# Optimization experiments

Hardware: AMD Instinct MI355X
Metric: run time of the kernel (lower is better)

Reference implementation:

```python
import jax, jax.numpy as jnp
import numpy as np

N = 3600      # nodes (pinned by h0/c0 shape in the torch module)
H = 512       # lstm_hidden
PES = 588     # pes feature width (LSTM input size)
PROT = 384    # protein feature width
OC = 256      # out_channels
E = 230400    # edges (avg degree 64)


def _lstm_cell(x, h, c, wih, whh, bih, bhh):
    # single-timestep PyTorch LSTM cell; gate order i, f, g, o
    g = x @ wih.T + h @ whh.T + bih + bhh
    i, f, gg, o = jnp.split(g, 4, axis=-1)
    c2 = jax.nn.sigmoid(f) * c + jax.nn.sigmoid(i) * jnp.tanh(gg)
    return jax.nn.sigmoid(o) * jnp.tanh(c2)


def _gcn(x, rows, cols, norm, W, b):
    # PyG GCNConv: X' = D^{-1/2}(A+I)D^{-1/2} X W + b
    xw = x @ W
    return jax.ops.segment_sum(xw[rows] * norm[:, None], cols, num_segments=N) + b


def setup_inputs() -> dict:
    key = jax.random.key(0)
    ks = jax.random.split(key, 24)
    s = 0.05
    d = {
        "x": jax.random.normal(ks[0], (N, PES + PROT), jnp.float32),
        "edge_index": jax.random.randint(ks[1], (2, E), 0, N),
        "h0": jax.random.normal(ks[2], (4, N, H), jnp.float32),
        "c0": jax.random.normal(ks[3], (4, N, H), jnp.float32),
    }
    ins = [PES, PES, 2 * H, 2 * H]
    names = ["l0f", "l0b", "l1f", "l1b"]
    for i, (nm, di) in enumerate(zip(names, ins)):
        d["wih" + nm] = jax.random.normal(ks[4 + 4 * i], (4 * H, di), jnp.float32) * s
        d["whh" + nm] = jax.random.normal(ks[5 + 4 * i], (4 * H, H), jnp.float32) * s
        d["bih" + nm] = jnp.zeros((4 * H,), jnp.float32)
        d["bhh" + nm] = jnp.zeros((4 * H,), jnp.float32)
    d["W1"] = jax.random.normal(ks[20], (PROT + 2 * H, 2 * OC), jnp.float32) * s
    d["b1"] = jnp.zeros((2 * OC,), jnp.float32)
    d["W2"] = jax.random.normal(ks[21], (2 * OC, OC), jnp.float32) * s
    d["b2"] = jnp.zeros((OC,), jnp.float32)
    return d


def reference(x, edge_index, h0, c0,
              wihl0f, whhl0f, bihl0f, bhhl0f,
              wihl0b, whhl0b, bihl0b, bhhl0b,
              wihl1f, whhl1f, bihl1f, bhhl1f,
              wihl1b, whhl1b, bihl1b, bhhl1b,
              W1, b1, W2, b2):
    pes = x[:, :PES]
    prot = x[:, PES:]
    # BiLSTM over seq_len=1: one cell step per direction per layer
    hf = _lstm_cell(pes, h0[0], c0[0], wihl0f, whhl0f, bihl0f, bhhl0f)
    hb = _lstm_cell(pes, h0[1], c0[1], wihl0b, whhl0b, bihl0b, bhhl0b)
    x1 = jnp.concatenate([hf, hb], axis=1)
    hf2 = _lstm_cell(x1, h0[2], c0[2], wihl1f, whhl1f, bihl1f, bhhl1f)
    hb2 = _lstm_cell(x1, h0[3], c0[3], wihl1b, whhl1b, bihl1b, bhhl1b)
    x_p = jnp.concatenate([hf2, hb2], axis=1) / 100.0
    feat = jnp.concatenate([prot, x_p], axis=1)  # dropout is identity in eval
    # add self-loops, symmetric normalization
    loop = jnp.arange(N)
    rows = jnp.concatenate([edge_index[0], loop])
    cols = jnp.concatenate([edge_index[1], loop])
    deg = jax.ops.segment_sum(jnp.ones_like(rows, jnp.float32), cols, num_segments=N)
    dinv = jax.lax.rsqrt(deg)  # deg >= 1 because of self-loops
    norm = dinv[rows] * dinv[cols]
    h1 = jax.nn.relu(_gcn(feat, rows, cols, norm, W1, b1))
    return _gcn(h1, rows, cols, norm, W2, b2)
```

## Files before the change

kernel.cpp:

```cpp
#include <hip/hip_runtime.h>
#include <hip/hip_bf16.h>

#define NN 3600
#define MP 3712
#define KADJ 3616
#define NH (3600*512)
#define EE 230400
#define NKT0 9
#define NKT1 12

typedef __hip_bfloat16 bf16;
typedef __bf16 bf16x8 __attribute__((ext_vector_type(8)));
typedef float f32x4 __attribute__((ext_vector_type(4)));
typedef int i32x8 __attribute__((ext_vector_type(8)));
typedef unsigned char u8x16 __attribute__((ext_vector_type(16)));

typedef __attribute__((address_space(1))) void as1v;
typedef __attribute__((address_space(3))) void as3v;

__device__ __forceinline__ void glds16(void* lds, const void* g) {
  __builtin_amdgcn_global_load_lds((as1v*)(void*)g, (as3v*)lds, 16, 0, 0);
}

__device__ __forceinline__ float sigm(float v) { return 1.0f / (1.0f + expf(-v)); }

__device__ __forceinline__ unsigned char f2fp8(float f) {
  return (unsigned char)(__builtin_amdgcn_cvt_pk_fp8_f32(f, 0.f, 0, false) & 0xff);
}

template<int MODE>
__global__ __launch_bounds__(256) void gemm_lstm8(
    const unsigned char* __restrict__ Axf, const unsigned char* __restrict__ Ahf,
    const unsigned char* __restrict__ Bf,
    const float* __restrict__ c0f, const float* __restrict__ bihf,
    const float* __restrict__ bhhf,
    const unsigned char* __restrict__ Axb, const unsigned char* __restrict__ Ahb,
    const unsigned char* __restrict__ Bb,
    const float* __restrict__ c0b, const float* __restrict__ bihb,
    const float* __restrict__ bhhb,
    void* __restrict__ dst1,
    int nktx, int nkt, int hx)
{
  __shared__ alignas(16) unsigned char smem[65536];
  const int hid = (int)blockIdx.y * 32 + (int)blockIdx.x;
  const int xcd = hid & 7, idx = hid >> 3;
  int bx, by;
  if (idx < 112) { bx = (xcd & 3) * 8 + (idx & 7); by = (xcd >> 2) * 14 + (idx >> 3); }
  else { int k = idx - 112; bx = (xcd & 3) * 8 + k * 2 + (xcd >> 2); by = 28; }
  const bool back = bx >= hx;
  const unsigned char* Ax = back ? Axb : Axf;
  const unsigned char* Ah = back ? Ahb : Ahf;
  const unsigned char* B  = back ? Bb  : Bf;
  const float* c0  = back ? c0b : c0f;
  const float* bih = back ? bihb : bihf;
  const float* bhh = back ? bhhb : bhhf;
  const int t = threadIdx.x, w = t >> 6, l = t & 63;
  const int nblk = back ? bx - hx : bx;
  const unsigned char* gA  = Ax + (((size_t)by * nktx) << 14) + t*16;
  const unsigned char* gAh = Ah + (((size_t)by * (nkt - nktx)) << 14) + t*16;
  const unsigned char* gB  = B  + (((size_t)nblk * nkt) << 14) + t*16;
  const int wm = (w>>1)*64, wn = (w&1)*64;
  const int kb = l >> 4;
  const int aoff = kb*4096 + (wm + (l&15))*32;
  const int boff = 16384 + kb*4096 + (wn + (l&15))*32;
  f32x4 acc[4][4] = {};

  auto STAGE = [&](int buf, int kt) {
    unsigned char* lA = smem + buf*32768 + w*1024;
    unsigned char* lB = smem + buf*32768 + 16384 + w*1024;
    const unsigned char* srcA = (kt < nktx) ? gA + ((size_t)kt << 14)
                                            : gAh + ((size_t)(kt - nktx) << 14);
    const size_t ko = (size_t)kt << 14;
    glds16(lA,          srcA);
    glds16(lA + 4096,   srcA + 4096);
    glds16(lA + 8192,   srcA + 8192);
    glds16(lA + 12288,  srcA + 12288);
    glds16(lB,          gB + ko);
    glds16(lB + 4096,   gB + ko + 4096);
    glds16(lB + 8192,   gB + ko + 8192);
    glds16(lB + 12288,  gB + ko + 12288);
  };

  STAGE(0, 0);
  STAGE(1, 1);
  int cur = 0;
  for (int kt = 0; kt < nkt; ++kt) {
    if (kt + 1 < nkt) asm volatile("s_waitcnt vmcnt(8)" ::: "memory");
    else              asm volatile("s_waitcnt vmcnt(0)" ::: "memory");
    __builtin_amdgcn_sched_barrier(0);
    __builtin_amdgcn_s_barrier();
    __builtin_amdgcn_sched_barrier(0);
    const unsigned char* base = smem + cur*32768;
    i32x8 av[4], bv[4];
#pragma unroll
    for (int mi = 0; mi < 4; ++mi) av[mi] = *(const i32x8*)(base + aoff + mi*512);
#pragma unroll
    for (int ni = 0; ni < 4; ++ni) bv[ni] = *(const i32x8*)(base + boff + ni*512);
#pragma unroll
    for (int mi = 0; mi < 4; ++mi)
#pragma unroll
      for (int ni = 0; ni < 4; ++ni)
        acc[mi][ni] = __builtin_amdgcn_mfma_scale_f32_16x16x128_f8f6f4(
            av[mi], bv[ni], acc[mi][ni], 0, 0, 0, 127, 0, 127);
    __builtin_amdgcn_sched_barrier(0);
    __builtin_amdgcn_s_barrier();
    __builtin_amdgcn_sched_barrier(0);
    if (kt + 2 < nkt) STAGE(cur, kt + 2);
    cur ^= 1;
  }
  const int jh = (((nblk << 7) + wn) >> 2) + (l & 15);
  const float bI = bih[jh]        + bhh[jh];
  const float bF = bih[512 + jh]  + bhh[512 + jh];
  const float bG = bih[1024 + jh] + bhh[1024 + jh];
  const float bO = bih[1536 + jh] + bhh[1536 + jh];
  const int crow = (by << 7) + wm + ((l>>4)<<2);
  const int kk = (back ? 512 : 0) + jh;
  const size_t kpart = ((size_t)(kk >> 7) << 14) + ((size_t)((kk >> 5) & 3) << 12) + (kk & 31);
  const int colOff = back ? 896 : 384;
#pragma unroll
  for (int mi = 0; mi < 4; ++mi)
#pragma unroll
    for (int jr = 0; jr < 4; ++jr) {
      const int n = crow + mi*16 + jr;
      if (n < NN) {
        const float gi = acc[mi][0][jr] + bI;
        const float gf = acc[mi][1][jr] + bF;
        const float gg = acc[mi][2][jr] + bG;
        const float go = acc[mi][3][jr] + bO;
        const float c2 = sigm(gf) * c0[(size_t)n*512 + jh] + sigm(gi) * tanhf(gg);
        const float h  = sigm(go) * tanhf(c2);
        if (MODE == 0) {
          const size_t off = (((size_t)(n >> 7) * 8) << 14) + kpart + ((size_t)(n & 127) << 5);
          ((unsigned char*)dst1)[off] = f2fp8(h);
        } else {
          ((bf16*)dst1)[(size_t)n*1408 + colOff + jh] = __float2bfloat16(h * 0.01f);
        }
      }
    }
}

__global__ __launch_bounds__(256) void gemm_bt_sk(const bf16* __restrict__ A,
                                                  const bf16* __restrict__ B,
                                                  float* __restrict__ Cp,
                                                  int Kp, int ldc, int ksteps)
{
  __shared__ alignas(16) char smem[32768];
  const int t = threadIdx.x, w = t >> 6, l = t & 63;
  const int mbase = blockIdx.y << 7, nbase = blockIdx.x << 7;
  const int total = Kp >> 5;
  const int kstart = blockIdx.z * ksteps;
  int steps = total - kstart; if (steps > ksteps) steps = ksteps;
  const size_t ldb = (size_t)Kp * 2;
  const char* gA = (const char*)A + (size_t)(mbase + w*16 + (l>>2)) * ldb
                   + (size_t)((l&3)*16) + (size_t)kstart*64;
  const char* gB = (const char*)B + (size_t)(nbase + w*16 + (l>>2)) * ldb
                   + (size_t)((l&3)*16) + (size_t)kstart*64;
  const int wm = (w>>1)*64, wn = (w&1)*64;
  const int aoff = (wm + (l&15))*64 + (l>>4)*16;
  const int boff = 8192 + (wn + (l&15))*64 + (l>>4)*16;
  f32x4 acc[4][4] = {};
  const size_t chunk = ldb * 64;

  auto STAGE = [&](int buf, int kt) {
    char* lA = smem + buf*16384 + w*1024;
    char* lB = smem + buf*16384 + 8192 + w*1024;
    const size_t ko = (size_t)kt * 64;
    glds16(lA,        gA + ko);
    glds16(lA + 4096, gA + ko + chunk);
    glds16(lB,        gB + ko);
    glds16(lB + 4096, gB + ko + chunk);
  };

  STAGE(0, 0);
  if (steps > 1) STAGE(1, 1);
  int cur = 0;
  for (int kt = 0; kt < steps; ++kt) {
    if (kt + 1 < steps) asm volatile("s_waitcnt vmcnt(4)" ::: "memory");
    else                asm volatile("s_waitcnt vmcnt(0)" ::: "memory");
    __builtin_amdgcn_sched_barrier(0);
    __builtin_amdgcn_s_barrier();
    __builtin_amdgcn_sched_barrier(0);
    const char* base = smem + cur*16384;
    bf16x8 av[4], bv[4];
#pragma unroll
    for (int mi = 0; mi < 4; ++mi) av[mi] = *(const bf16x8*)(base + aoff + mi*1024);
#pragma unroll
    for (int ni = 0; ni < 4; ++ni) bv[ni] = *(const bf16x8*)(base + boff + ni*1024);
#pragma unroll
    for (int mi = 0; mi < 4; ++mi)
#pragma unroll
      for (int ni = 0; ni < 4; ++ni)
        acc[mi][ni] = __builtin_amdgcn_mfma_f32_16x16x32_bf16(av[mi], bv[ni], acc[mi][ni], 0, 0, 0);
    __builtin_amdgcn_sched_barrier(0);
    __builtin_amdgcn_s_barrier();
    __builtin_amdgcn_sched_barrier(0);
    if (kt + 2 < steps) STAGE(cur, kt + 2);
    cur ^= 1;
  }
  float* Cz = Cp + (size_t)blockIdx.z * ((size_t)(gridDim.y << 7) * ldc);
  const int crow = mbase + wm + ((l>>4)<<2);
  const int ccol = nbase + wn + (l&15);
#pragma unroll
  for (int mi = 0; mi < 4; ++mi)
#pragma unroll
    for (int ni = 0; ni < 4; ++ni) {
      float* cp = Cz + (size_t)(crow + mi*16)*ldc + (ccol + ni*16);
#pragma unroll
      for (int j = 0; j < 4; ++j) cp[(size_t)j*ldc] = acc[mi][ni][j];
    }
}

__global__ void reduce_bf_pad(const float* __restrict__ p, bf16* __restrict__ dst, int Z)
{
  int k = blockIdx.x*256 + threadIdx.x;
  int r = blockIdx.y;
  if (k >= KADJ) return;
  const size_t psz = (size_t)gridDim.y * MP;
  float s = 0.f;
  if (k < NN)
    for (int z = 0; z < Z; ++z) s += p[(size_t)z*psz + (size_t)r*MP + k];
  dst[(size_t)r*KADJ + k] = __float2bfloat16(s);
}

__global__ void reduce_relu_bf(const float* __restrict__ p, const float* __restrict__ b,
                               bf16* __restrict__ dst)
{
  int idx = blockIdx.x*256 + threadIdx.x;
  int f = idx & 511;
  float s = b[f];
#pragma unroll
  for (int z = 0; z < 4; ++z) s += p[(size_t)z*MP*512 + idx];
  dst[idx] = __float2bfloat16(fmaxf(s, 0.f));
}

__global__ void reduce_bias_out(const float* __restrict__ p, const float* __restrict__ b,
                                float* __restrict__ out)
{
  int idx = blockIdx.x*256 + threadIdx.x;
  if (idx >= NN*256) return;
  int f = idx & 255;
  float s = b[f];
#pragma unroll
  for (int z = 0; z < 8; ++z) s += p[(size_t)z*MP*256 + idx];
  out[idx] = s;
}

__global__ void pack_B_8(const float* __restrict__ wih, const float* __restrict__ whh,
                         unsigned char* __restrict__ dst, int kx, int nkt)
{
  const int kt = blockIdx.x >> 2, kbId = blockIdx.x & 3;
  const int t = threadIdx.x;
  const int r = t >> 1, kio = (t & 1) << 4;
  const int R = ((int)blockIdx.y << 7) + r;
  const int src = (((R >> 4) & 3) << 9) + ((R >> 6) << 4) + (R & 15);
  const int kbase = kt*128 + kbId*32 + kio;
  u8x16 v;
#pragma unroll
  for (int i = 0; i < 16; ++i) {
    const int k = kbase + i;
    float f = 0.f;
    if (k < kx) f = wih[(size_t)src*kx + k];
    else if (k < kx + 512) f = whh[(size_t)src*512 + (k - kx)];
    v[i] = f2fp8(f);
  }
  *(u8x16*)(dst + (((size_t)blockIdx.y*nkt + kt) << 14) + (kbId << 12) + (r << 5) + kio) = v;
}

__global__ void pack_A0_8(const float* __restrict__ x, const float* __restrict__ h0,
                          unsigned char* __restrict__ a0f, unsigned char* __restrict__ a0b)
{
  const int kt = blockIdx.x >> 2, kbId = blockIdx.x & 3;
  const int t = threadIdx.x;
  const int r = t >> 1, kio = (t & 1) << 4;
  const int n = ((int)blockIdx.y << 7) + r;
  const int kbase = kt*128 + kbId*32 + kio;
  const float* hsrc = h0 + (size_t)blockIdx.z * NH;
  u8x16 v;
#pragma unroll
  for (int i = 0; i < 16; ++i) {
    const int k = kbase + i;
    float f = 0.f;
    if (n < NN) {
      if (k < 588) f = x[(size_t)n*972 + k];
      else if (k < 1100) f = hsrc[(size_t)n*512 + (k - 588)];
    }
    v[i] = f2fp8(f);
  }
  unsigned char* dst = blockIdx.z ? a0b : a0f;
  *(u8x16*)(dst + (((size_t)blockIdx.y*NKT0 + kt) << 14) + (kbId << 12) + (r << 5) + kio) = v;
}

__global__ void pack_A1h_8(const float* __restrict__ h0,
                           unsigned char* __restrict__ ahf, unsigned char* __restrict__ ahb)
{
  const int ktl = blockIdx.x >> 2, kbId = blockIdx.x & 3;
  const int t = threadIdx.x;
  const int r = t >> 1, kio = (t & 1) << 4;
  const int n = ((int)blockIdx.y << 7) + r;
  const int kbase = ktl*128 + kbId*32 + kio;
  const float* hsrc = h0 + (size_t)(2 + blockIdx.z) * NH;
  u8x16 v;
#pragma unroll
  for (int i = 0; i < 16; ++i) {
    const int k = kbase + i;
    float f = (n < NN) ? hsrc[(size_t)n*512 + k] : 0.f;
    v[i] = f2fp8(f);
  }
  unsigned char* dst = blockIdx.z ? ahb : ahf;
  *(u8x16*)(dst + (((size_t)blockIdx.y*4 + ktl) << 14) + (kbId << 12) + (r << 5) + kio) = v;
}

__global__ void pack_BT(const float* __restrict__ W, bf16* __restrict__ dst, int Nc, int K)
{
  int k = blockIdx.x*256 + threadIdx.x;
  int n = blockIdx.y;
  if (k >= K) return;
  dst[(size_t)n*K + k] = __float2bfloat16(W[(size_t)k*Nc + n]);
}

__global__ void pack_prot(const float* __restrict__ x, bf16* __restrict__ afeat)
{
  int k = blockIdx.x*256 + threadIdx.x;
  int n = blockIdx.y;
  if (k >= 384) return;
  float v = (n < NN) ? x[(size_t)n*972 + 588 + k] : 0.f;
  afeat[(size_t)n*1408 + k] = __float2bfloat16(v);
}

__global__ void deg_count(const int* __restrict__ ecols, int* __restrict__ deg)
{
  int e = blockIdx.x*256 + threadIdx.x;
  if (e < EE) atomicAdd(&deg[ecols[e]], 1);
}

__global__ void calc_dinv(const int* __restrict__ deg, float* __restrict__ dinv)
{
  int n = blockIdx.x*256 + threadIdx.x;
  if (n < NN) dinv[n] = 1.0f / sqrtf((float)(deg[n] + 1));
}

__global__ void adj_scatter(const int* __restrict__ er, const int* __restrict__ ec,
                            const float* __restrict__ dinv, float* __restrict__ adjf)
{
  int e = blockIdx.x*256 + threadIdx.x;
  if (e < EE) {
    int r = er[e], c = ec[e];
    atomicAdd(&adjf[(size_t)c*KADJ + r], dinv[r]*dinv[c]);
  } else if (e < EE + NN) {
    int n = e - EE;
    float d = dinv[n];
    atomicAdd(&adjf[(size_t)n*KADJ + n], d*d);
  }
}

__global__ void cvt_bf(const float* __restrict__ src, int lds,
                       bf16* __restrict__ dst, int rv, int kv)
{
  int k = blockIdx.x*256 + threadIdx.x;
  int r = blockIdx.y;
  if (k >= KADJ) return;
  float v = (r < rv && k < kv) ? src[(size_t)r*lds + k] : 0.f;
  dst[(size_t)r*KADJ + k] = __float2bfloat16(v);
}

#define OFF_DEG   ((size_t)0)
#define OFF_DINV  ((size_t)16384)
#define OFF_BW2   ((size_t)32768)
#define OFF_B0F   ((size_t)294912)
#define OFF_B0B   ((size_t)4882432)
#define OFF_B1F   ((size_t)9469952)
#define OFF_B1B   ((size_t)15761408)
#define OFF_BW1   ((size_t)22052864)
#define OFF_A0F   ((size_t)23494656)
#define OFF_A0B   ((size_t)31809536)
#define OFF_A1X   ((size_t)40124416)
#define OFF_A1HF  ((size_t)43925504)
#define OFF_A1HB  ((size_t)45826048)
#define OFF_G     ((size_t)62930944)
#define OFF_AFEAT OFF_A0F
#define OFF_XW1P  OFF_G
#define OFF_XWT1B OFF_B0F
#define OFF_ADJF  ((size_t)40124416)
#define OFF_ADJB  ((size_t)4194304)
#define OFF_H1P   ((size_t)40124416)
#define OFF_H1    ((size_t)70533120)
#define OFF_XW2P  ((size_t)74334208)
#define OFF_XWT2B ((size_t)89538560)
#define OFF_O2P   ((size_t)40124416)

extern "C" void kernel_launch(void* const* d_in, const int* in_sizes, int n_in,
                              void* d_out, int out_size, void* d_ws, size_t ws_size,
                              hipStream_t stream)
{
  const float* x    = (const float*)d_in[0];
  const int*   ei   = (const int*)d_in[1];
  const float* h0   = (const float*)d_in[2];
  const float* c0   = (const float*)d_in[3];
  const float* wih0f = (const float*)d_in[4];
  const float* whh0f = (const float*)d_in[5];
  const float* bih0f = (const float*)d_in[6];
  const float* bhh0f = (const float*)d_in[7];
  const float* wih0b = (const float*)d_in[8];
  const float* whh0b = (const float*)d_in[9];
  const float* bih0b = (const float*)d_in[10];
  const float* bhh0b = (const float*)d_in[11];
  const float* wih1f = (const float*)d_in[12];
  const float* whh1f = (const float*)d_in[13];
  const float* bih1f = (const float*)d_in[14];
  const float* bhh1f = (const float*)d_in[15];
  const float* wih1b = (const float*)d_in[16];
  const float* whh1b = (const float*)d_in[17];
  const float* bih1b = (const float*)d_in[18];
  const float* bhh1b = (const float*)d_in[19];
  const float* W1 = (const float*)d_in[20];
  const float* b1 = (const float*)d_in[21];
  const float* W2 = (const float*)d_in[22];
  const float* b2 = (const float*)d_in[23];

  char* ws = (char*)d_ws;
  int*   deg  = (int*)(ws + OFF_DEG);
  float* dinv = (float*)(ws + OFF_DINV);
  unsigned char* B0f8 = (unsigned char*)(ws + OFF_B0F);
  unsigned char* B0b8 = (unsigned char*)(ws + OFF_B0B);
  unsigned char* B1f8 = (unsigned char*)(ws + OFF_B1F);
  unsigned char* B1b8 = (unsigned char*)(ws + OFF_B1B);
  bf16* BW1 = (bf16*)(ws + OFF_BW1);
  bf16* BW2 = (bf16*)(ws + OFF_BW2);
  unsigned char* A0f8 = (unsigned char*)(ws + OFF_A0F);
  unsigned char* A0b8 = (unsigned char*)(ws + OFF_A0B);
  unsigned char* A1X8 = (unsigned char*)(ws + OFF_A1X);
  unsigned char* A1HF = (unsigned char*)(ws + OFF_A1HF);
  unsigned char* A1HB = (unsigned char*)(ws + OFF_A1HB);
  bf16* Afeat = (bf16*)(ws + OFF_AFEAT);
  float* xw1p  = (float*)(ws + OFF_XW1P);
  bf16*  xwt1b = (bf16*)(ws + OFF_XWT1B);
  float* adjf  = (float*)(ws + OFF_ADJF);
  bf16*  adjb  = (bf16*)(ws + OFF_ADJB);
  float* h1p   = (float*)(ws + OFF_H1P);
  bf16*  h1bf  = (bf16*)(ws + OFF_H1);
  float* xw2p  = (float*)(ws + OFF_XW2P);
  bf16*  xwt2b = (bf16*)(ws + OFF_XWT2B);
  float* o2p   = (float*)(ws + OFF_O2P);
  float* outp = (float*)d_out;

  hipMemsetAsync(deg, 0, (size_t)NN*4, stream);
  deg_count<<<dim3((EE+255)/256), 256, 0, stream>>>(ei + EE, deg);
  calc_dinv<<<dim3(15), 256, 0, stream>>>(deg, dinv);

  pack_B_8<<<dim3(NKT0*4, 16), 256, 0, stream>>>(wih0f, whh0f, B0f8, 588, NKT0);
  pack_B_8<<<dim3(NKT0*4, 16), 256, 0, stream>>>(wih0b, whh0b, B0b8, 588, NKT0);
  pack_B_8<<<dim3(NKT1*4, 16), 256, 0, stream>>>(wih1f, whh1f, B1f8, 1024, NKT1);
  pack_B_8<<<dim3(NKT1*4, 16), 256, 0, stream>>>(wih1b, whh1b, B1b8, 1024, NKT1);
  pack_BT<<<dim3(6, 512), 256, 0, stream>>>(W1, BW1, 512, 1408);
  pack_BT<<<dim3(2, 256), 256, 0, stream>>>(W2, BW2, 256, 512);

  pack_A0_8<<<dim3(NKT0*4, 29, 2), 256, 0, stream>>>(x, h0, A0f8, A0b8);
  pack_A1h_8<<<dim3(16, 29, 2), 256, 0, stream>>>(h0, A1HF, A1HB);

  gemm_lstm8<0><<<dim3(32, 29), 256, 0, stream>>>(
      A0f8, A0f8, B0f8, c0,              bih0f, bhh0f,
      A0b8, A0b8, B0b8, c0 + (size_t)NH, bih0b, bhh0b,
      A1X8, NKT0, NKT0, 16);

  pack_prot<<<dim3(2, MP), 256, 0, stream>>>(x, Afeat);

  gemm_lstm8<1><<<dim3(32, 29), 256, 0, stream>>>(
      A1X8, A1HF, B1f8, c0 + (size_t)2*NH, bih1f, bhh1f,
      A1X8, A1HB, B1b8, c0 + (size_t)3*NH, bih1b, bhh1b,
      Afeat, 8, NKT1, 16);

  gemm_bt_sk<<<dim3(29, 4, 4), 256, 0, stream>>>(BW1, Afeat, xw1p, 1408, MP, 11);
  reduce_bf_pad<<<dim3(15, 512), 256, 0, stream>>>(xw1p, xwt1b, 4);

  hipMemsetAsync(adjf, 0, (size_t)NN*KADJ*4, stream);
  adj_scatter<<<dim3((EE+NN+255)/256), 256, 0, stream>>>(ei, ei + EE, dinv, adjf);
  cvt_bf<<<dim3(15, MP), 256, 0, stream>>>(adjf, KADJ, adjb, NN, KADJ);

  gemm_bt_sk<<<dim3(4, 29, 4), 256, 0, stream>>>(adjb, xwt1b, h1p, KADJ, 512, 29);
  reduce_relu_bf<<<dim3(MP*512/256), 256, 0, stream>>>(h1p, b1, h1bf);

  gemm_bt_sk<<<dim3(29, 2, 4), 256, 0, stream>>>(BW2, h1bf, xw2p, 512, MP, 4);
  reduce_bf_pad<<<dim3(15, 256), 256, 0, stream>>>(xw2p, xwt2b, 4);

  gemm_bt_sk<<<dim3(2, 29, 8), 256, 0, stream>>>(adjb, xwt2b, o2p, KADJ, 256, 15);
  reduce_bias_out<<<dim3(3600), 256, 0, stream>>>(o2p, b2, outp);
}
```

Before: 329.5 us.

## Load GEMM fragments directly from global into registers, dropping LDS staging

```diff
diff --git a/kernel.cpp b/kernel.cpp
--- a/kernel.cpp
+++ b/kernel.cpp
@@ -15,13 +15,6 @@
 typedef int i32x8 __attribute__((ext_vector_type(8)));
 typedef unsigned char u8x16 __attribute__((ext_vector_type(16)));
 
-typedef __attribute__((address_space(1))) void as1v;
-typedef __attribute__((address_space(3))) void as3v;
-
-__device__ __forceinline__ void glds16(void* lds, const void* g) {
-  __builtin_amdgcn_global_load_lds((as1v*)(void*)g, (as3v*)lds, 16, 0, 0);
-}
-
 __device__ __forceinline__ float sigm(float v) { return 1.0f / (1.0f + expf(-v)); }
 
 __device__ __forceinline__ unsigned char f2fp8(float f) {
@@ -29,7 +22,7 @@
 }
 
 template<int MODE>
-__global__ __launch_bounds__(256) void gemm_lstm8(
+__global__ __launch_bounds__(256, 2) void gemm_lstm8(
     const unsigned char* __restrict__ Axf, const unsigned char* __restrict__ Ahf,
     const unsigned char* __restrict__ Bf,
     const float* __restrict__ c0f, const float* __restrict__ bihf,
@@ -41,7 +34,6 @@
     void* __restrict__ dst1,
     int nktx, int nkt, int hx)
 {
-  __shared__ alignas(16) unsigned char smem[65536];
   const int hid = (int)blockIdx.y * 32 + (int)blockIdx.x;
   const int xcd = hid & 7, idx = hid >> 3;
   int bx, by;
@@ -56,58 +48,39 @@
   const float* bhh = back ? bhhb : bhhf;
   const int t = threadIdx.x, w = t >> 6, l = t & 63;
   const int nblk = back ? bx - hx : bx;
-  const unsigned char* gA  = Ax + (((size_t)by * nktx) << 14) + t*16;
-  const unsigned char* gAh = Ah + (((size_t)by * (nkt - nktx)) << 14) + t*16;
-  const unsigned char* gB  = B  + (((size_t)nblk * nkt) << 14) + t*16;
   const int wm = (w>>1)*64, wn = (w&1)*64;
   const int kb = l >> 4;
-  const int aoff = kb*4096 + (wm + (l&15))*32;
-  const int boff = 16384 + kb*4096 + (wn + (l&15))*32;
+  const int afr = kb*4096 + (wm + (l&15))*32;
+  const int bfr = kb*4096 + (wn + (l&15))*32;
+  const unsigned char* gAx = Ax + (((size_t)by * nktx) << 14) + afr;
+  const unsigned char* gAh = Ah + (((size_t)by * (nkt - nktx)) << 14) + afr;
+  const unsigned char* gB  = B  + (((size_t)nblk * nkt) << 14) + bfr;
   f32x4 acc[4][4] = {};
-
-  auto STAGE = [&](int buf, int kt) {
-    unsigned char* lA = smem + buf*32768 + w*1024;
-    unsigned char* lB = smem + buf*32768 + 16384 + w*1024;
-    const unsigned char* srcA = (kt < nktx) ? gA + ((size_t)kt << 14)
-                                            : gAh + ((size_t)(kt - nktx) << 14);
-    const size_t ko = (size_t)kt << 14;
-    glds16(lA,          srcA);
-    glds16(lA + 4096,   srcA + 4096);
-    glds16(lA + 8192,   srcA + 8192);
-    glds16(lA + 12288,  srcA + 12288);
-    glds16(lB,          gB + ko);
-    glds16(lB + 4096,   gB + ko + 4096);
-    glds16(lB + 8192,   gB + ko + 8192);
-    glds16(lB + 12288,  gB + ko + 12288);
-  };
-
-  STAGE(0, 0);
-  STAGE(1, 1);
-  int cur = 0;
-  for (int kt = 0; kt < nkt; ++kt) {
-    if (kt + 1 < nkt) asm volatile("s_waitcnt vmcnt(8)" ::: "memory");
-    else              asm volatile("s_waitcnt vmcnt(0)" ::: "memory");
-    __builtin_amdgcn_sched_barrier(0);
-    __builtin_amdgcn_s_barrier();
-    __builtin_amdgcn_sched_barrier(0);
-    const unsigned char* base = smem + cur*32768;
-    i32x8 av[4], bv[4];
-#pragma unroll
-    for (int mi = 0; mi < 4; ++mi) av[mi] = *(const i32x8*)(base + aoff + mi*512);
-#pragma unroll
-    for (int ni = 0; ni < 4; ++ni) bv[ni] = *(const i32x8*)(base + boff + ni*512);
-#pragma unroll
-    for (int mi = 0; mi < 4; ++mi)
-#pragma unroll
-      for (int ni = 0; ni < 4; ++ni)
-        acc[mi][ni] = __builtin_amdgcn_mfma_scale_f32_16x16x128_f8f6f4(
-            av[mi], bv[ni], acc[mi][ni], 0, 0, 0, 127, 0, 127);
-    __builtin_amdgcn_sched_barrier(0);
-    __builtin_amdgcn_s_barrier();
-    __builtin_amdgcn_sched_barrier(0);
-    if (kt + 2 < nkt) STAGE(cur, kt + 2);
-    cur ^= 1;
-  }
+  i32x8 av0[4], bv0[4], av1[4], bv1[4];
+
+#define LOADF8(AV, BV, KT) { \
+  const unsigned char* sA = ((KT) < nktx) ? gAx + ((size_t)(KT) << 14) \
+                                          : gAh + ((size_t)((KT) - nktx) << 14); \
+  const unsigned char* sB = gB + ((size_t)(KT) << 14); \
+  _Pragma("unroll") for (int mi = 0; mi < 4; ++mi) AV[mi] = *(const i32x8*)(sA + mi*512); \
+  _Pragma("unroll") for (int ni = 0; ni < 4; ++ni) BV[ni] = *(const i32x8*)(sB + ni*512); }
+
+#define MFMA8(AV, BV) { \
+  _Pragma("unroll") for (int mi = 0; mi < 4; ++mi) \
+  _Pragma("unroll") for (int ni = 0; ni < 4; ++ni) \
+    acc[mi][ni] = __builtin_amdgcn_mfma_scale_f32_16x16x128_f8f6f4( \
+        AV[mi], BV[ni], acc[mi][ni], 0, 0, 0, 127, 0, 127); }
+
+  LOADF8(av0, bv0, 0);
+  for (int kt = 0; kt < nkt; kt += 2) {
+    if (kt + 1 < nkt) LOADF8(av1, bv1, kt + 1);
+    MFMA8(av0, bv0);
+    if (kt + 2 < nkt) LOADF8(av0, bv0, kt + 2);
+    if (kt + 1 < nkt) MFMA8(av1, bv1);
+  }
+#undef LOADF8
+#undef MFMA8
+
   const int jh = (((nblk << 7) + wn) >> 2) + (l & 15);
   const float bI = bih[jh]        + bhh[jh];
   const float bF = bih[512 + jh]  + bhh[512 + jh];
@@ -144,59 +117,40 @@
                                                   float* __restrict__ Cp,
                                                   int Kp, int ldc, int ksteps)
 {
-  __shared__ alignas(16) char smem[32768];
   const int t = threadIdx.x, w = t >> 6, l = t & 63;
   const int mbase = blockIdx.y << 7, nbase = blockIdx.x << 7;
   const int total = Kp >> 5;
   const int kstart = blockIdx.z * ksteps;
   int steps = total - kstart; if (steps > ksteps) steps = ksteps;
   const size_t ldb = (size_t)Kp * 2;
-  const char* gA = (const char*)A + (size_t)(mbase + w*16 + (l>>2)) * ldb
-                   + (size_t)((l&3)*16) + (size_t)kstart*64;
-  const char* gB = (const char*)B + (size_t)(nbase + w*16 + (l>>2)) * ldb
-                   + (size_t)((l&3)*16) + (size_t)kstart*64;
   const int wm = (w>>1)*64, wn = (w&1)*64;
-  const int aoff = (wm + (l&15))*64 + (l>>4)*16;
-  const int boff = 8192 + (wn + (l&15))*64 + (l>>4)*16;
+  const char* gA = (const char*)A + (size_t)(mbase + wm + (l&15)) * ldb
+                   + (size_t)((l>>4)*16) + (size_t)kstart*64;
+  const char* gB = (const char*)B + (size_t)(nbase + wn + (l&15)) * ldb
+                   + (size_t)((l>>4)*16) + (size_t)kstart*64;
   f32x4 acc[4][4] = {};
-  const size_t chunk = ldb * 64;
-
-  auto STAGE = [&](int buf, int kt) {
-    char* lA = smem + buf*16384 + w*1024;
-    char* lB = smem + buf*16384 + 8192 + w*1024;
-    const size_t ko = (size_t)kt * 64;
-    glds16(lA,        gA + ko);
-    glds16(lA + 4096, gA + ko + chunk);
-    glds16(lB,        gB + ko);
-    glds16(lB + 4096, gB + ko + chunk);
-  };
-
-  STAGE(0, 0);
-  if (steps > 1) STAGE(1, 1);
-  int cur = 0;
-  for (int kt = 0; kt < steps; ++kt) {
-    if (kt + 1 < steps) asm volatile("s_waitcnt vmcnt(4)" ::: "memory");
-    else                asm volatile("s_waitcnt vmcnt(0)" ::: "memory");
-    __builtin_amdgcn_sched_barrier(0);
-    __builtin_amdgcn_s_barrier();
-    __builtin_amdgcn_sched_barrier(0);
-    const char* base = smem + cur*16384;
-    bf16x8 av[4], bv[4];
-#pragma unroll
-    for (int mi = 0; mi < 4; ++mi) av[mi] = *(const bf16x8*)(base + aoff + mi*1024);
-#pragma unroll
-    for (int ni = 0; ni < 4; ++ni) bv[ni] = *(const bf16x8*)(base + boff + ni*1024);
-#pragma unroll
-    for (int mi = 0; mi < 4; ++mi)
-#pragma unroll
-      for (int ni = 0; ni < 4; ++ni)
-        acc[mi][ni] = __builtin_amdgcn_mfma_f32_16x16x32_bf16(av[mi], bv[ni], acc[mi][ni], 0, 0, 0);
-    __builtin_amdgcn_sched_barrier(0);
-    __builtin_amdgcn_s_barrier();
-    __builtin_amdgcn_sched_barrier(0);
-    if (kt + 2 < steps) STAGE(cur, kt + 2);
-    cur ^= 1;
-  }
+  bf16x8 av0[4], bv0[4], av1[4], bv1[4];
+
+#define LOADFB(AV, BV, KT) { \
+  const size_t ko = (size_t)(KT) * 64; \
+  _Pragma("unroll") for (int mi = 0; mi < 4; ++mi) AV[mi] = *(const bf16x8*)(gA + ko + (size_t)mi*16*ldb); \
+  _Pragma("unroll") for (int ni = 0; ni < 4; ++ni) BV[ni] = *(const bf16x8*)(gB + ko + (size_t)ni*16*ldb); }
+
+#define MFMAB(AV, BV) { \
+  _Pragma("unroll") for (int mi = 0; mi < 4; ++mi) \
+  _Pragma("unroll") for (int ni = 0; ni < 4; ++ni) \
+    acc[mi][ni] = __builtin_amdgcn_mfma_f32_16x16x32_bf16(AV[mi], BV[ni], acc[mi][ni], 0, 0, 0); }
+
+  LOADFB(av0, bv0, 0);
+  for (int kt = 0; kt < steps; kt += 2) {
+    if (kt + 1 < steps) LOADFB(av1, bv1, kt + 1);
+    MFMAB(av0, bv0);
+    if (kt + 2 < steps) LOADFB(av0, bv0, kt + 2);
+    if (kt + 1 < steps) MFMAB(av1, bv1);
+  }
+#undef LOADFB
+#undef MFMAB
+
   float* Cz = Cp + (size_t)blockIdx.z * ((size_t)(gridDim.y << 7) * ldc);
   const int crow = mbase + wm + ((l>>4)<<2);
   const int ccol = nbase + wn + (l&15);
```

New measurement: 392.7 us. 1.19x slower.

## Enlarge LSTM FP8 GEMM tiles to 256x256 with 512-thread blocks

Applied to the files above, without the earlier changes.

```diff
diff --git a/kernel.cpp b/kernel.cpp
--- a/kernel.cpp
+++ b/kernel.cpp
@@ -29,7 +29,7 @@
 }
 
 template<int MODE>
-__global__ __launch_bounds__(256) void gemm_lstm8(
+__global__ __launch_bounds__(512, 2) void gemm_lstm8(
     const unsigned char* __restrict__ Axf, const unsigned char* __restrict__ Ahf,
     const unsigned char* __restrict__ Bf,
     const float* __restrict__ c0f, const float* __restrict__ bihf,
@@ -41,12 +41,10 @@
     void* __restrict__ dst1,
     int nktx, int nkt, int hx)
 {
-  __shared__ alignas(16) unsigned char smem[65536];
-  const int hid = (int)blockIdx.y * 32 + (int)blockIdx.x;
-  const int xcd = hid & 7, idx = hid >> 3;
-  int bx, by;
-  if (idx < 112) { bx = (xcd & 3) * 8 + (idx & 7); by = (xcd >> 2) * 14 + (idx >> 3); }
-  else { int k = idx - 112; bx = (xcd & 3) * 8 + k * 2 + (xcd >> 2); by = 28; }
+  __shared__ alignas(16) unsigned char smem[131072];
+  const int hid = (int)blockIdx.y * 16 + (int)blockIdx.x;
+  const int swz = (hid & 7) * 30 + (hid >> 3);
+  const int bx = swz & 15, by = swz >> 4;
   const bool back = bx >= hx;
   const unsigned char* Ax = back ? Axb : Axf;
   const unsigned char* Ah = back ? Ahb : Ahf;
@@ -55,30 +53,35 @@
   const float* bih = back ? bihb : bihf;
   const float* bhh = back ? bhhb : bhhf;
   const int t = threadIdx.x, w = t >> 6, l = t & 63;
+  const int wr = w >> 1, wc = w & 1;
   const int nblk = back ? bx - hx : bx;
-  const unsigned char* gA  = Ax + (((size_t)by * nktx) << 14) + t*16;
-  const unsigned char* gAh = Ah + (((size_t)by * (nkt - nktx)) << 14) + t*16;
-  const unsigned char* gB  = B  + (((size_t)nblk * nkt) << 14) + t*16;
-  const int wm = (w>>1)*64, wn = (w&1)*64;
+  const int nkth = nkt - nktx;
+  const unsigned char* gAx0 = Ax + (((size_t)(2*by)   * nktx) << 14);
+  const unsigned char* gAx1 = Ax + (((size_t)(2*by+1) * nktx) << 14);
+  const unsigned char* gAh0 = Ah + (((size_t)(2*by)   * nkth) << 14);
+  const unsigned char* gAh1 = Ah + (((size_t)(2*by+1) * nkth) << 14);
+  const unsigned char* gB0  = B  + (((size_t)(2*nblk)   * nkt) << 14);
+  const unsigned char* gB1  = B  + (((size_t)(2*nblk+1) * nkt) << 14);
   const int kb = l >> 4;
-  const int aoff = kb*4096 + (wm + (l&15))*32;
-  const int boff = 16384 + kb*4096 + (wn + (l&15))*32;
-  f32x4 acc[4][4] = {};
+  const int aoff = (wr >> 1) * 16384 + kb*4096 + ((wr & 1)*64 + (l & 15))*32;
+  const int boff = 32768 + wc*16384 + kb*4096 + (l & 15)*32;
+  f32x4 acc[4][8] = {};
 
   auto STAGE = [&](int buf, int kt) {
-    unsigned char* lA = smem + buf*32768 + w*1024;
-    unsigned char* lB = smem + buf*32768 + 16384 + w*1024;
-    const unsigned char* srcA = (kt < nktx) ? gA + ((size_t)kt << 14)
-                                            : gAh + ((size_t)(kt - nktx) << 14);
-    const size_t ko = (size_t)kt << 14;
-    glds16(lA,          srcA);
-    glds16(lA + 4096,   srcA + 4096);
-    glds16(lA + 8192,   srcA + 8192);
-    glds16(lA + 12288,  srcA + 12288);
-    glds16(lB,          gB + ko);
-    glds16(lB + 4096,   gB + ko + 4096);
-    glds16(lB + 8192,   gB + ko + 8192);
-    glds16(lB + 12288,  gB + ko + 12288);
+    unsigned char* ld = smem + buf*65536;
+    const unsigned char *sA0, *sA1;
+    if (kt < nktx) { sA0 = gAx0 + ((size_t)kt << 14); sA1 = gAx1 + ((size_t)kt << 14); }
+    else { sA0 = gAh0 + ((size_t)(kt - nktx) << 14); sA1 = gAh1 + ((size_t)(kt - nktx) << 14); }
+    const unsigned char* sB0 = gB0 + ((size_t)kt << 14);
+    const unsigned char* sB1 = gB1 + ((size_t)kt << 14);
+    glds16(ld + t*16,          sA0 + t*16);
+    glds16(ld + 8192 + t*16,   sA0 + 8192 + t*16);
+    glds16(ld + 16384 + t*16,  sA1 + t*16);
+    glds16(ld + 24576 + t*16,  sA1 + 8192 + t*16);
+    glds16(ld + 32768 + t*16,  sB0 + t*16);
+    glds16(ld + 40960 + t*16,  sB0 + 8192 + t*16);
+    glds16(ld + 49152 + t*16,  sB1 + t*16);
+    glds16(ld + 57344 + t*16,  sB1 + 8192 + t*16);
   };
 
   STAGE(0, 0);
@@ -90,53 +93,57 @@
     __builtin_amdgcn_sched_barrier(0);
     __builtin_amdgcn_s_barrier();
     __builtin_amdgcn_sched_barrier(0);
-    const unsigned char* base = smem + cur*32768;
-    i32x8 av[4], bv[4];
-#pragma unroll
-    for (int mi = 0; mi < 4; ++mi) av[mi] = *(const i32x8*)(base + aoff + mi*512);
-#pragma unroll
-    for (int ni = 0; ni < 4; ++ni) bv[ni] = *(const i32x8*)(base + boff + ni*512);
-#pragma unroll
-    for (int mi = 0; mi < 4; ++mi)
-#pragma unroll
-      for (int ni = 0; ni < 4; ++ni)
-        acc[mi][ni] = __builtin_amdgcn_mfma_scale_f32_16x16x128_f8f6f4(
-            av[mi], bv[ni], acc[mi][ni], 0, 0, 0, 127, 0, 127);
+    const unsigned char* base = smem + cur*65536;
+    i32x8 a4[4];
+#pragma unroll
+    for (int mi = 0; mi < 4; ++mi) a4[mi] = *(const i32x8*)(base + aoff + mi*512);
+#pragma unroll
+    for (int nf = 0; nf < 8; ++nf) {
+      const i32x8 bfr = *(const i32x8*)(base + boff + nf*512);
+#pragma unroll
+      for (int mi = 0; mi < 4; ++mi)
+        acc[mi][nf] = __builtin_amdgcn_mfma_scale_f32_16x16x128_f8f6f4(
+            a4[mi], bfr, acc[mi][nf], 0, 0, 0, 127, 0, 127);
+    }
     __builtin_amdgcn_sched_barrier(0);
     __builtin_amdgcn_s_barrier();
     __builtin_amdgcn_sched_barrier(0);
     if (kt + 2 < nkt) STAGE(cur, kt + 2);
     cur ^= 1;
   }
-  const int jh = (((nblk << 7) + wn) >> 2) + (l & 15);
-  const float bI = bih[jh]        + bhh[jh];
-  const float bF = bih[512 + jh]  + bhh[512 + jh];
-  const float bG = bih[1024 + jh] + bhh[1024 + jh];
-  const float bO = bih[1536 + jh] + bhh[1536 + jh];
-  const int crow = (by << 7) + wm + ((l>>4)<<2);
-  const int kk = (back ? 512 : 0) + jh;
-  const size_t kpart = ((size_t)(kk >> 7) << 14) + ((size_t)((kk >> 5) & 3) << 12) + (kk & 31);
-  const int colOff = back ? 896 : 384;
-#pragma unroll
-  for (int mi = 0; mi < 4; ++mi)
-#pragma unroll
-    for (int jr = 0; jr < 4; ++jr) {
-      const int n = crow + mi*16 + jr;
-      if (n < NN) {
-        const float gi = acc[mi][0][jr] + bI;
-        const float gf = acc[mi][1][jr] + bF;
-        const float gg = acc[mi][2][jr] + bG;
-        const float go = acc[mi][3][jr] + bO;
-        const float c2 = sigm(gf) * c0[(size_t)n*512 + jh] + sigm(gi) * tanhf(gg);
-        const float h  = sigm(go) * tanhf(c2);
-        if (MODE == 0) {
-          const size_t off = (((size_t)(n >> 7) * 8) << 14) + kpart + ((size_t)(n & 127) << 5);
-          ((unsigned char*)dst1)[off] = f2fp8(h);
-        } else {
-          ((bf16*)dst1)[(size_t)n*1408 + colOff + jh] = __float2bfloat16(h * 0.01f);
+  const int crow = by*256 + wr*64 + ((l >> 4) << 2);
+  const int jbase = (nblk*4 + wc*2) * 16 + (l & 15);
+#pragma unroll
+  for (int ng = 0; ng < 2; ++ng) {
+    const int jh = jbase + ng*16;
+    const float bI = bih[jh]        + bhh[jh];
+    const float bF = bih[512 + jh]  + bhh[512 + jh];
+    const float bG = bih[1024 + jh] + bhh[1024 + jh];
+    const float bO = bih[1536 + jh] + bhh[1536 + jh];
+    const int kk = (back ? 512 : 0) + jh;
+    const size_t kpart = ((size_t)(kk >> 7) << 14) + ((size_t)((kk >> 5) & 3) << 12) + (kk & 31);
+    const int colOff = back ? 896 : 384;
+#pragma unroll
+    for (int mi = 0; mi < 4; ++mi)
+#pragma unroll
+      for (int jr = 0; jr < 4; ++jr) {
+        const int n = crow + mi*16 + jr;
+        if (n < NN) {
+          const float gi = acc[mi][ng*4 + 0][jr] + bI;
+          const float gf = acc[mi][ng*4 + 1][jr] + bF;
+          const float gg = acc[mi][ng*4 + 2][jr] + bG;
+          const float go = acc[mi][ng*4 + 3][jr] + bO;
+          const float c2 = sigm(gf) * c0[(size_t)n*512 + jh] + sigm(gi) * tanhf(gg);
+          const float h  = sigm(go) * tanhf(c2);
+          if (MODE == 0) {
+            const size_t off = (((size_t)(n >> 7) * 8) << 14) + kpart + ((size_t)(n & 127) << 5);
+            ((unsigned char*)dst1)[off] = f2fp8(h);
+          } else {
+            ((bf16*)dst1)[(size_t)n*1408 + colOff + jh] = __float2bfloat16(h * 0.01f);
+          }
         }
       }
-    }
+  }
 }
 
 __global__ __launch_bounds__(256) void gemm_bt_sk(const bf16* __restrict__ A,
@@ -374,8 +381,8 @@
 #define OFF_A0F   ((size_t)23494656)
 #define OFF_A0B   ((size_t)31809536)
 #define OFF_A1X   ((size_t)40124416)
-#define OFF_A1HF  ((size_t)43925504)
-#define OFF_A1HB  ((size_t)45826048)
+#define OFF_A1HF  ((size_t)44056576)
+#define OFF_A1HB  ((size_t)46022656)
 #define OFF_G     ((size_t)62930944)
 #define OFF_AFEAT OFF_A0F
 #define OFF_XW1P  OFF_G
@@ -454,20 +461,20 @@
   pack_BT<<<dim3(6, 512), 256, 0, stream>>>(W1, BW1, 512, 1408);
   pack_BT<<<dim3(2, 256), 256, 0, stream>>>(W2, BW2, 256, 512);
 
-  pack_A0_8<<<dim3(NKT0*4, 29, 2), 256, 0, stream>>>(x, h0, A0f8, A0b8);
-  pack_A1h_8<<<dim3(16, 29, 2), 256, 0, stream>>>(h0, A1HF, A1HB);
-
-  gemm_lstm8<0><<<dim3(32, 29), 256, 0, stream>>>(
+  pack_A0_8<<<dim3(NKT0*4, 30, 2), 256, 0, stream>>>(x, h0, A0f8, A0b8);
+  pack_A1h_8<<<dim3(16, 30, 2), 256, 0, stream>>>(h0, A1HF, A1HB);
+
+  gemm_lstm8<0><<<dim3(16, 15), 512, 0, stream>>>(
       A0f8, A0f8, B0f8, c0,              bih0f, bhh0f,
       A0b8, A0b8, B0b8, c0 + (size_t)NH, bih0b, bhh0b,
-      A1X8, NKT0, NKT0, 16);
+      A1X8, NKT0, NKT0, 8);
 
   pack_prot<<<dim3(2, MP), 256, 0, stream>>>(x, Afeat);
 
-  gemm_lstm8<1><<<dim3(32, 29), 256, 0, stream>>>(
+  gemm_lstm8<1><<<dim3(16, 15), 512, 0, stream>>>(
       A1X8, A1HF, B1f8, c0 + (size_t)2*NH, bih1f, bhh1f,
       A1X8, A1HB, B1b8, c0 + (size_t)3*NH, bih1b, bhh1b,
-      Afeat, 8, NKT1, 16);
+      Afeat, 8, NKT1, 8);
 
   gemm_bt_sk<<<dim3(29, 4, 4), 256, 0, stream>>>(BW1, Afeat, xw1p, 1408, MP, 11);
   reduce_bf_pad<<<dim3(15, 512), 256, 0, stream>>>(xw1p, xwt1b, 4);
```

After: 422.6 us. 28.3% more time.

## Scatter adjacency directly into bf16 via CAS and merge pack kernels

Applied to the files above, without the earlier changes.

```diff
diff --git a/kernel.cpp b/kernel.cpp
--- a/kernel.cpp
+++ b/kernel.cpp
@@ -26,6 +26,15 @@
 
 __device__ __forceinline__ unsigned char f2fp8(float f) {
   return (unsigned char)(__builtin_amdgcn_cvt_pk_fp8_f32(f, 0.f, 0, false) & 0xff);
+}
+
+__device__ __forceinline__ unsigned short f2bf_bits(float f) {
+  __hip_bfloat16 h = __float2bfloat16(f);
+  return *reinterpret_cast<unsigned short*>(&h);
+}
+__device__ __forceinline__ float bf_bits2f(unsigned short u) {
+  __hip_bfloat16 h; *reinterpret_cast<unsigned short*>(&h) = u;
+  return __bfloat162float(h);
 }
 
 template<int MODE>
@@ -245,9 +254,20 @@
   out[idx] = s;
 }
 
-__global__ void pack_B_8(const float* __restrict__ wih, const float* __restrict__ whh,
-                         unsigned char* __restrict__ dst, int kx, int nkt)
-{
+__global__ void pack_B8_all(const float* __restrict__ wih0f, const float* __restrict__ whh0f,
+                            const float* __restrict__ wih0b, const float* __restrict__ whh0b,
+                            const float* __restrict__ wih1f, const float* __restrict__ whh1f,
+                            const float* __restrict__ wih1b, const float* __restrict__ whh1b,
+                            unsigned char* __restrict__ B0f, unsigned char* __restrict__ B0b,
+                            unsigned char* __restrict__ B1f, unsigned char* __restrict__ B1b)
+{
+  const int z = blockIdx.z;
+  const float* wih; const float* whh; unsigned char* dst; int kx, nkt;
+  if      (z == 0) { wih = wih0f; whh = whh0f; dst = B0f; kx = 588;  nkt = NKT0; }
+  else if (z == 1) { wih = wih0b; whh = whh0b; dst = B0b; kx = 588;  nkt = NKT0; }
+  else if (z == 2) { wih = wih1f; whh = whh1f; dst = B1f; kx = 1024; nkt = NKT1; }
+  else             { wih = wih1b; whh = whh1b; dst = B1b; kx = 1024; nkt = NKT1; }
+  if ((int)blockIdx.x >= nkt*4) return;
   const int kt = blockIdx.x >> 2, kbId = blockIdx.x & 3;
   const int t = threadIdx.x;
   const int r = t >> 1, kio = (t & 1) << 4;
@@ -266,52 +286,56 @@
   *(u8x16*)(dst + (((size_t)blockIdx.y*nkt + kt) << 14) + (kbId << 12) + (r << 5) + kio) = v;
 }
 
-__global__ void pack_A0_8(const float* __restrict__ x, const float* __restrict__ h0,
-                          unsigned char* __restrict__ a0f, unsigned char* __restrict__ a0b)
-{
-  const int kt = blockIdx.x >> 2, kbId = blockIdx.x & 3;
+__global__ void pack_A8_all(const float* __restrict__ x, const float* __restrict__ h0,
+                            unsigned char* __restrict__ a0f, unsigned char* __restrict__ a0b,
+                            unsigned char* __restrict__ ahf, unsigned char* __restrict__ ahb)
+{
+  const int z = blockIdx.z;
   const int t = threadIdx.x;
   const int r = t >> 1, kio = (t & 1) << 4;
   const int n = ((int)blockIdx.y << 7) + r;
-  const int kbase = kt*128 + kbId*32 + kio;
-  const float* hsrc = h0 + (size_t)blockIdx.z * NH;
-  u8x16 v;
-#pragma unroll
-  for (int i = 0; i < 16; ++i) {
-    const int k = kbase + i;
-    float f = 0.f;
-    if (n < NN) {
-      if (k < 588) f = x[(size_t)n*972 + k];
-      else if (k < 1100) f = hsrc[(size_t)n*512 + (k - 588)];
+  if (z < 2) {
+    const int kt = blockIdx.x >> 2, kbId = blockIdx.x & 3;
+    const int kbase = kt*128 + kbId*32 + kio;
+    const float* hsrc = h0 + (size_t)z * NH;
+    u8x16 v;
+#pragma unroll
+    for (int i = 0; i < 16; ++i) {
+      const int k = kbase + i;
+      float f = 0.f;
+      if (n < NN) {
+        if (k < 588) f = x[(size_t)n*972 + k];
+        else if (k < 1100) f = hsrc[(size_t)n*512 + (k - 588)];
+      }
+      v[i] = f2fp8(f);
     }
-    v[i] = f2fp8(f);
+    unsigned char* dst = z ? a0b : a0f;
+    *(u8x16*)(dst + (((size_t)blockIdx.y*NKT0 + kt) << 14) + (kbId << 12) + (r << 5) + kio) = v;
+  } else {
+    if ((int)blockIdx.x >= 16) return;
+    const int ktl = blockIdx.x >> 2, kbId = blockIdx.x & 3;
+    const int kbase = ktl*128 + kbId*32 + kio;
+    const float* hsrc = h0 + (size_t)(z) * NH;
+    u8x16 v;
+#pragma unroll
+    for (int i = 0; i < 16; ++i) {
+      const int k = kbase + i;
+      float f = (n < NN) ? hsrc[(size_t)n*512 + k] : 0.f;
+      v[i] = f2fp8(f);
+    }
+    unsigned char* dst = (z == 3) ? ahb : ahf;
+    *(u8x16*)(dst + (((size_t)blockIdx.y*4 + ktl) << 14) + (kbId << 12) + (r << 5) + kio) = v;
   }
-  unsigned char* dst = blockIdx.z ? a0b : a0f;
-  *(u8x16*)(dst + (((size_t)blockIdx.y*NKT0 + kt) << 14) + (kbId << 12) + (r << 5) + kio) = v;
-}
-
-__global__ void pack_A1h_8(const float* __restrict__ h0,
-                           unsigned char* __restrict__ ahf, unsigned char* __restrict__ ahb)
-{
-  const int ktl = blockIdx.x >> 2, kbId = blockIdx.x & 3;
-  const int t = threadIdx.x;
-  const int r = t >> 1, kio = (t & 1) << 4;
-  const int n = ((int)blockIdx.y << 7) + r;
-  const int kbase = ktl*128 + kbId*32 + kio;
-  const float* hsrc = h0 + (size_t)(2 + blockIdx.z) * NH;
-  u8x16 v;
-#pragma unroll
-  for (int i = 0; i < 16; ++i) {
-    const int k = kbase + i;
-    float f = (n < NN) ? hsrc[(size_t)n*512 + k] : 0.f;
-    v[i] = f2fp8(f);
-  }
-  unsigned char* dst = blockIdx.z ? ahb : ahf;
-  *(u8x16*)(dst + (((size_t)blockIdx.y*4 + ktl) << 14) + (kbId << 12) + (r << 5) + kio) = v;
-}
-
-__global__ void pack_BT(const float* __restrict__ W, bf16* __restrict__ dst, int Nc, int K)
-{
+}
+
+__global__ void pack_BT_all(const float* __restrict__ W1, bf16* __restrict__ BW1,
+                            const float* __restrict__ W2, bf16* __restrict__ BW2)
+{
+  const int z = blockIdx.z;
+  const float* W; bf16* dst; int Nc, K, nx, ny;
+  if (z == 0) { W = W1; dst = BW1; Nc = 512; K = 1408; nx = 6; ny = 512; }
+  else        { W = W2; dst = BW2; Nc = 256; K = 512;  nx = 2; ny = 256; }
+  if ((int)blockIdx.x >= nx || (int)blockIdx.y >= ny) return;
   int k = blockIdx.x*256 + threadIdx.x;
   int n = blockIdx.y;
   if (k >= K) return;
@@ -339,28 +363,28 @@
   if (n < NN) dinv[n] = 1.0f / sqrtf((float)(deg[n] + 1));
 }
 
-__global__ void adj_scatter(const int* __restrict__ er, const int* __restrict__ ec,
-                            const float* __restrict__ dinv, float* __restrict__ adjf)
+__global__ void adj_scatter_bf(const int* __restrict__ er, const int* __restrict__ ec,
+                               const float* __restrict__ dinv,
+                               unsigned int* __restrict__ adjw)
 {
   int e = blockIdx.x*256 + threadIdx.x;
-  if (e < EE) {
-    int r = er[e], c = ec[e];
-    atomicAdd(&adjf[(size_t)c*KADJ + r], dinv[r]*dinv[c]);
-  } else if (e < EE + NN) {
-    int n = e - EE;
-    float d = dinv[n];
-    atomicAdd(&adjf[(size_t)n*KADJ + n], d*d);
-  }
-}
-
-__global__ void cvt_bf(const float* __restrict__ src, int lds,
-                       bf16* __restrict__ dst, int rv, int kv)
-{
-  int k = blockIdx.x*256 + threadIdx.x;
-  int r = blockIdx.y;
-  if (k >= KADJ) return;
-  float v = (r < rv && k < kv) ? src[(size_t)r*lds + k] : 0.f;
-  dst[(size_t)r*KADJ + k] = __float2bfloat16(v);
+  int r, c; float v;
+  if (e < EE)            { r = er[e]; c = ec[e]; v = dinv[r]*dinv[c]; }
+  else if (e < EE + NN)  { r = c = e - EE; float d = dinv[r]; v = d*d; }
+  else return;
+  unsigned int* p = adjw + ((size_t)c*KADJ + r) / 2;
+  const bool hi = (r & 1) != 0;
+  unsigned int old = *p, assumed;
+  do {
+    assumed = old;
+    unsigned short h = hi ? (unsigned short)(assumed >> 16)
+                          : (unsigned short)(assumed & 0xffffu);
+    unsigned short nh = f2bf_bits(bf_bits2f(h) + v);
+    unsigned int nw = hi ? ((assumed & 0x0000ffffu) | ((unsigned int)nh << 16))
+                         : ((assumed & 0xffff0000u) | (unsigned int)nh);
+    if (nw == assumed) break;
+    old = atomicCAS(p, assumed, nw);
+  } while (old != assumed);
 }
 
 #define OFF_DEG   ((size_t)0)
@@ -380,7 +404,6 @@
 #define OFF_AFEAT OFF_A0F
 #define OFF_XW1P  OFF_G
 #define OFF_XWT1B OFF_B0F
-#define OFF_ADJF  ((size_t)40124416)
 #define OFF_ADJB  ((size_t)4194304)
 #define OFF_H1P   ((size_t)40124416)
 #define OFF_H1    ((size_t)70533120)
@@ -434,7 +457,6 @@
   bf16* Afeat = (bf16*)(ws + OFF_AFEAT);
   float* xw1p  = (float*)(ws + OFF_XW1P);
   bf16*  xwt1b = (bf16*)(ws + OFF_XWT1B);
-  float* adjf  = (float*)(ws + OFF_ADJF);
   bf16*  adjb  = (bf16*)(ws + OFF_ADJB);
   float* h1p   = (float*)(ws + OFF_H1P);
   bf16*  h1bf  = (bf16*)(ws + OFF_H1);
@@ -447,15 +469,12 @@
   deg_count<<<dim3((EE+255)/256), 256, 0, stream>>>(ei + EE, deg);
   calc_dinv<<<dim3(15), 256, 0, stream>>>(deg, dinv);
 
-  pack_B_8<<<dim3(NKT0*4, 16), 256, 0, stream>>>(wih0f, whh0f, B0f8, 588, NKT0);
-  pack_B_8<<<dim3(NKT0*4, 16), 256, 0, stream>>>(wih0b, whh0b, B0b8, 588, NKT0);
-  pack_B_8<<<dim3(NKT1*4, 16), 256, 0, stream>>>(wih1f, whh1f, B1f8, 1024, NKT1);
-  pack_B_8<<<dim3(NKT1*4, 16), 256, 0, stream>>>(wih1b, whh1b, B1b8, 1024, NKT1);
-  pack_BT<<<dim3(6, 512), 256, 0, stream>>>(W1, BW1, 512, 1408);
-  pack_BT<<<dim3(2, 256), 256, 0, stream>>>(W2, BW2, 256, 512);
-
-  pack_A0_8<<<dim3(NKT0*4, 29, 2), 256, 0, stream>>>(x, h0, A0f8, A0b8);
-  pack_A1h_8<<<dim3(16, 29, 2), 256, 0, stream>>>(h0, A1HF, A1HB);
+  pack_B8_all<<<dim3(NKT1*4, 16, 4), 256, 0, stream>>>(
+      wih0f, whh0f, wih0b, whh0b, wih1f, whh1f, wih1b, whh1b,
+      B0f8, B0b8, B1f8, B1b8);
+  pack_BT_all<<<dim3(6, 512, 2), 256, 0, stream>>>(W1, BW1, W2, BW2);
+
+  pack_A8_all<<<dim3(NKT0*4, 29, 4), 256, 0, stream>>>(x, h0, A0f8, A0b8, A1HF, A1HB);
 
   gemm_lstm8<0><<<dim3(32, 29), 256, 0, stream>>>(
       A0f8, A0f8, B0f8, c0,              bih0f, bhh0f,
@@ -472,9 +491,9 @@
   gemm_bt_sk<<<dim3(29, 4, 4), 256, 0, stream>>>(BW1, Afeat, xw1p, 1408, MP, 11);
   reduce_bf_pad<<<dim3(15, 512), 256, 0, stream>>>(xw1p, xwt1b, 4);
 
-  hipMemsetAsync(adjf, 0, (size_t)NN*KADJ*4, stream);
-  adj_scatter<<<dim3((EE+NN+255)/256), 256, 0, stream>>>(ei, ei + EE, dinv, adjf);
-  cvt_bf<<<dim3(15, MP), 256, 0, stream>>>(adjf, KADJ, adjb, NN, KADJ);
+  hipMemsetAsync(adjb, 0, (size_t)MP*KADJ*2, stream);
+  adj_scatter_bf<<<dim3((EE+NN+255)/256), 256, 0, stream>>>(
+      ei, ei + EE, dinv, (unsigned int*)adjb);
 
   gemm_bt_sk<<<dim3(4, 29, 4), 256, 0, stream>>>(adjb, xwt1b, h1p, KADJ, 512, 29);
   reduce_relu_bf<<<dim3(MP*512/256), 256, 0, stream>>>(h1p, b1, h1bf);
```

Result: faster. 297.0 us (-9.9%).
